# Kernel tuning notes

Measured on AMD Instinct MI355X. Metric: run time of the kernel, lower is better.

## Reference

```python
import jax, jax.numpy as jnp
import numpy as np

N_EMBD = 1024
HEAD_SIZE = 64  # n_embd // n_head = 1024 // 16


def setup_inputs() -> dict:
    key = jax.random.key(0)
    ks = jax.random.split(key, 7)
    B, T, C, H = 4, 2048, N_EMBD, HEAD_SIZE
    s = 1.0 / np.sqrt(C)
    return {
        "x": jax.random.normal(ks[0], (B, T, C), dtype=jnp.float32),
        "Wq": jax.random.normal(ks[1], (C, H), dtype=jnp.float32) * s,
        "bq": jax.random.normal(ks[2], (H,), dtype=jnp.float32) * 0.01,
        "Wk": jax.random.normal(ks[3], (C, H), dtype=jnp.float32) * s,
        "bk": jax.random.normal(ks[4], (H,), dtype=jnp.float32) * 0.01,
        "Wv": jax.random.normal(ks[5], (C, H), dtype=jnp.float32) * s,
        "bv": jax.random.normal(ks[6], (H,), dtype=jnp.float32) * 0.01,
    }


def reference(x, Wq, bq, Wk, bk, Wv, bv):
    # x: [B, T, C]
    B, T, C = x.shape
    q = x @ Wq + bq  # [B, T, H]
    k = x @ Wk + bk  # [B, T, H]
    v = x @ Wv + bv  # [B, T, H]
    # NOTE: original module does NOT scale by 1/sqrt(head_size)
    wei = jnp.einsum("bth,bsh->bts", q, k)  # [B, T, T]
    causal = jnp.tril(jnp.ones((T, T), dtype=bool))
    wei = jnp.where(causal, wei, -jnp.inf)
    wei = jax.nn.softmax(wei, axis=-1)
    out = jnp.einsum("bts,bsh->bth", wei, v)  # [B, T, H]
    return out
```

## Files before the change

kernel.cpp:

```cpp
#include <hip/hip_runtime.h>

typedef float f32x4 __attribute__((ext_vector_type(4)));
typedef short s16x4 __attribute__((ext_vector_type(4)));
typedef short s16x8 __attribute__((ext_vector_type(8)));

#define LOG2E 1.4426950408889634f

__device__ __forceinline__ short f2bf(float f) {
  unsigned u = __float_as_uint(f);
  unsigned r = (u + 0x7fffu + ((u >> 16) & 1u)) >> 16;
  return (short)r;
}
__device__ __forceinline__ float bf2f(short s) {
  return __uint_as_float(((unsigned)(unsigned short)s) << 16);
}
__device__ __forceinline__ unsigned cvt_pk_bf16(float a, float b) {
  unsigned r;
  asm("v_cvt_pk_bf16_f32 %0, %1, %2" : "=v"(r) : "v"(a), "v"(b));
  return r;
}

__device__ __forceinline__ f32x4 mfma16(s16x4 a, s16x4 b, f32x4 c) {
  return __builtin_amdgcn_mfma_f32_16x16x16bf16_1k(a, b, c, 0, 0, 0);
}
__device__ __forceinline__ f32x4 mfma32(s16x8 a, s16x8 b, f32x4 c) {
  return __builtin_amdgcn_mfma_f32_16x16x32_bf16(a, b, c, 0, 0, 0);
}

__device__ __forceinline__ void gl_lds16(const void* gp, void* sp) {
  __builtin_amdgcn_global_load_lds(
      (__attribute__((address_space(1))) void*)const_cast<void*>(gp),
      (__attribute__((address_space(3))) void*)sp, 16, 0, 0);
}

__global__ __launch_bounds__(256) void prep_w(
    const float* __restrict__ Wq, const float* __restrict__ Wk, const float* __restrict__ Wv,
    short* __restrict__ wt_hi, short* __restrict__ wt_lo) {
  int idx = blockIdx.x * 256 + threadIdx.x;
  int n = idx >> 10;
  int c = idx & 1023;
  const float* W = (n < 64) ? Wq : ((n < 128) ? Wk : Wv);
  float v = W[c * 64 + (n & 63)];
  short hi = f2bf(v);
  short lo = f2bf(v - bf2f(hi));
  wt_hi[idx] = hi;
  wt_lo[idx] = lo;
}

__global__ __launch_bounds__(512, 2) void proj_qkv(
    const float* __restrict__ x,
    const short* __restrict__ wt_hi, const short* __restrict__ wt_lo,
    const float* __restrict__ bq, const float* __restrict__ bk, const float* __restrict__ bv,
    short* __restrict__ q_hi, short* __restrict__ q_lo,
    short* __restrict__ k_hi, short* __restrict__ k_lo,
    short* __restrict__ v_t) {
  const int tid = threadIdx.x;
  const int lane = tid & 63;
  const int wv = tid >> 6;
  const int col = lane & 15;
  const int g = lane >> 4;
  const int mg = wv >> 2;
  const int ng = wv & 3;
  const int tokbase = blockIdx.x * 32;

  __shared__ short lds[5][12288];

  const int wsl = ((lane & 3) ^ ((lane >> 3) & 3)) * 8;
  const short* s0 = wt_hi + (size_t)(16 * wv + (lane >> 2)) * 1024 + wsl;
  const int d0 = wv * 512;
  const int c1 = wv + 8;
  const short* s1 = (c1 < 12 ? wt_hi + (size_t)(16 * c1 + (lane >> 2)) * 1024
                             : wt_lo + (size_t)(16 * (c1 - 12) + (lane >> 2)) * 1024) + wsl;
  const int d1 = (c1 < 12) ? c1 * 512 : 6144 + (c1 - 12) * 512;
  const int c2 = wv + 16;
  const bool isx = (c2 >= 20);
  const short* s2 = isx
      ? (const short*)(x + (size_t)(tokbase + 8 * (c2 - 20) + (lane >> 3)) * 1024 +
                       ((lane & 7) ^ (lane >> 3)) * 4)
      : wt_lo + (size_t)(16 * (c2 - 12) + (lane >> 2)) * 1024 + wsl;
  const int d2 = isx ? 10240 + (c2 - 20) * 512 : 6144 + (c2 - 12) * 512;
  const int st2 = isx ? 64 : 32;

#define STAGE(BP, S) do { \
    gl_lds16(s0 + (S) * 32, (BP) + d0); \
    gl_lds16(s1 + (S) * 32, (BP) + d1); \
    gl_lds16(s2 + (S) * st2, (BP) + d2); \
  } while (0)

#define PIPE_WAIT(N) do { \
    asm volatile("s_waitcnt vmcnt(" #N ")" ::: "memory"); \
    __builtin_amdgcn_s_barrier(); \
    __builtin_amdgcn_sched_barrier(0); \
  } while (0)
#define PIPE_END do { \
    asm volatile("s_waitcnt lgkmcnt(0)" ::: "memory"); \
    __builtin_amdgcn_sched_barrier(0); \
    __builtin_amdgcn_s_barrier(); \
  } while (0)

  const int arow = mg * 16 + col;
  const int xq0 = ((2 * g) ^ (arow & 7)) << 2;
  const int xq1 = ((2 * g + 1) ^ (arow & 7)) << 2;
  const int rq = ng * 16 + col;
  const int ws = (g ^ ((rq >> 1) & 3)) << 3;

  f32x4 accQ = {0,0,0,0}, accK = {0,0,0,0}, accV = {0,0,0,0};

  typedef union { unsigned u[4]; s16x8 v8; } pk8;

#define COMPUTE(BP) do { \
    const short* bp_ = (BP); \
    const float* xb_ = (const float*)(bp_ + 10240); \
    f32x4 x0_ = *(const f32x4*)(xb_ + arow * 32 + xq0); \
    f32x4 x1_ = *(const f32x4*)(xb_ + arow * 32 + xq1); \
    pk8 xh_, xl_; \
    xh_.u[0] = cvt_pk_bf16(x0_[0], x0_[1]); \
    xh_.u[1] = cvt_pk_bf16(x0_[2], x0_[3]); \
    xh_.u[2] = cvt_pk_bf16(x1_[0], x1_[1]); \
    xh_.u[3] = cvt_pk_bf16(x1_[2], x1_[3]); \
    xl_.u[0] = cvt_pk_bf16(x0_[0] - __uint_as_float(xh_.u[0] << 16), \
                           x0_[1] - __uint_as_float(xh_.u[0] & 0xffff0000u)); \
    xl_.u[1] = cvt_pk_bf16(x0_[2] - __uint_as_float(xh_.u[1] << 16), \
                           x0_[3] - __uint_as_float(xh_.u[1] & 0xffff0000u)); \
    xl_.u[2] = cvt_pk_bf16(x1_[0] - __uint_as_float(xh_.u[2] << 16), \
                           x1_[1] - __uint_as_float(xh_.u[2] & 0xffff0000u)); \
    xl_.u[3] = cvt_pk_bf16(x1_[2] - __uint_as_float(xh_.u[3] << 16), \
                           x1_[3] - __uint_as_float(xh_.u[3] & 0xffff0000u)); \
    s16x8 qh_ = *(const s16x8*)(bp_ + rq * 32 + ws); \
    s16x8 kh_ = *(const s16x8*)(bp_ + (64 + rq) * 32 + ws); \
    s16x8 vh_ = *(const s16x8*)(bp_ + (128 + rq) * 32 + ws); \
    s16x8 ql_ = *(const s16x8*)(bp_ + 6144 + rq * 32 + ws); \
    s16x8 kl_ = *(const s16x8*)(bp_ + 6144 + (64 + rq) * 32 + ws); \
    accQ = mfma32(xh_.v8, qh_, accQ); \
    accK = mfma32(xh_.v8, kh_, accK); \
    accV = mfma32(xh_.v8, vh_, accV); \
    accQ = mfma32(xl_.v8, qh_, accQ); \
    accK = mfma32(xl_.v8, kh_, accK); \
    accQ = mfma32(xh_.v8, ql_, accQ); \
    accK = mfma32(xh_.v8, kl_, accK); \
  } while (0)

  short* cA = &lds[0][0];
  short* cB = &lds[1][0];
  short* cC = &lds[2][0];
  short* cD = &lds[3][0];
  short* cE = &lds[4][0];

  STAGE(cA, 0); STAGE(cB, 1); STAGE(cC, 2); STAGE(cD, 3);

#pragma unroll 1
  for (int b = 0; b < 28; ++b) {
    STAGE(cE, b + 4);
    PIPE_WAIT(12);
    COMPUTE(cA);
    PIPE_END;
    short* t = cA; cA = cB; cB = cC; cC = cD; cD = cE; cE = t;
  }
  PIPE_WAIT(9); COMPUTE(cA); PIPE_END;
  PIPE_WAIT(6); COMPUTE(cB); PIPE_END;
  PIPE_WAIT(3); COMPUTE(cC); PIPE_END;
  PIPE_WAIT(0); COMPUTE(cD);

  {
    const int hQ = ng * 16 + col;
    const float biasq = bq[hQ];
    const float biask = bk[hQ];
    const float biasv = bv[hQ];
#pragma unroll
    for (int r = 0; r < 4; ++r) {
      const int tok = tokbase + mg * 16 + 4 * g + r;
      float fq = accQ[r] + biasq;
      short qh = f2bf(fq);
      q_hi[(size_t)tok * 64 + hQ] = qh;
      q_lo[(size_t)tok * 64 + hQ] = f2bf(fq - bf2f(qh));
      float fk = accK[r] + biask;
      short kh = f2bf(fk);
      k_hi[(size_t)tok * 64 + hQ] = kh;
      k_lo[(size_t)tok * 64 + hQ] = f2bf(fk - bf2f(kh));
      const int bb = tok >> 11;
      const int tl = tok & 2047;
      v_t[((size_t)bb * 64 + hQ) * 2048 + tl] = f2bf(accV[r] + biasv);
    }
  }
#undef STAGE
#undef PIPE_WAIT
#undef PIPE_END
#undef COMPUTE
}

__global__ __launch_bounds__(512, 2) void attn(
    const short* __restrict__ q_hi, const short* __restrict__ q_lo,
    const short* __restrict__ k_hi, const short* __restrict__ k_lo,
    const short* __restrict__ v_t,
    float* __restrict__ pm, float* __restrict__ pl, float* __restrict__ pO) {
  const int tid = threadIdx.x;
  const int lane = tid & 63;
  const int w = tid >> 6;
  const int col = lane & 15;
  const int g = lane >> 4;
  const int bid = blockIdx.x;
  const int p = bid & 7;
  const int b = (bid >> 3) & 3;
  const int s = bid >> 5;
  if (s > p) return;

  __shared__ short lds[3][12288];

  const int qlo = 256 * p + 32 * w;
  const int kb0 = 256 * s;

  const short* qbh = q_hi + (size_t)(b * 2048 + qlo + col) * 64 + g * 8;
  const short* qbl = q_lo + (size_t)(b * 2048 + qlo + col) * 64 + g * 8;
  s16x8 qh0a = *(const s16x8*)(qbh);
  s16x8 qh1a = *(const s16x8*)(qbh + 32);
  s16x8 ql0a = *(const s16x8*)(qbl);
  s16x8 ql1a = *(const s16x8*)(qbl + 32);
  s16x8 qh0b = *(const s16x8*)(qbh + 16 * 64);
  s16x8 qh1b = *(const s16x8*)(qbh + 16 * 64 + 32);
  s16x8 ql0b = *(const s16x8*)(qbl + 16 * 64);
  s16x8 ql1b = *(const s16x8*)(qbl + 16 * 64 + 32);
  asm volatile("s_waitcnt vmcnt(0)" ::: "memory");
  __builtin_amdgcn_sched_barrier(0);

  f32x4 oA0 = {0,0,0,0}, oA1 = {0,0,0,0}, oA2 = {0,0,0,0}, oA3 = {0,0,0,0};
  f32x4 oB0 = {0,0,0,0}, oB1 = {0,0,0,0}, oB2 = {0,0,0,0}, oB3 = {0,0,0,0};
  float mA = -3.0e38f, lA = 0.0f, mB = -3.0e38f, lB = 0.0f;

#define STAGE(BP, J) do { \
    const int kbs_ = kb0 + 64 * (J); \
    const int r_ = 8 * w + (lane >> 3); \
    const int lc_ = (lane & 7) ^ (lane >> 3); \
    gl_lds16(k_hi + (size_t)(b * 2048 + kbs_ + r_) * 64 + lc_ * 8, (BP) + 8 * w * 64); \
    gl_lds16(k_lo + (size_t)(b * 2048 + kbs_ + r_) * 64 + lc_ * 8, (BP) + 4096 + 8 * w * 64); \
    gl_lds16(v_t + ((size_t)b * 64 + r_) * 2048 + kbs_ + lc_ * 8, (BP) + 8192 + 8 * w * 64); \
  } while (0)

#define PIPE_WAIT(N) do { \
    asm volatile("s_waitcnt vmcnt(" #N ")" ::: "memory"); \
    __builtin_amdgcn_s_barrier(); \
    __builtin_amdgcn_sched_barrier(0); \
  } while (0)
#define PIPE_END do { \
    asm volatile("s_waitcnt lgkmcnt(0)" ::: "memory"); \
    __builtin_amdgcn_sched_barrier(0); \
    __builtin_amdgcn_s_barrier(); \
  } while (0)

#define TILE_U(Qh0, Qh1, Ql0, Ql1, mX, lX, O0, O1, O2, O3, DIAG) do { \
    f32x4 u1_ = {0,0,0,0}, u2_ = {0,0,0,0}; \
    u1_ = mfma32(kh0_, Qh0, u1_); u1_ = mfma32(kh1_, Qh1, u1_); \
    u2_ = mfma32(kh0_, Ql0, u2_); u2_ = mfma32(kh1_, Ql1, u2_); \
    u2_ = mfma32(kl0_, Qh0, u2_); u2_ = mfma32(kl1_, Qh1, u2_); \
    f32x4 s_ = u1_ + u2_; \
    if (kg0_ == (DIAG)) { \
      _Pragma("unroll") for (int i = 0; i < 4; ++i) \
        if (4 * g + i > col) s_[i] = -3.0e38f; \
    } \
    float mx_ = fmaxf(fmaxf(s_[0], s_[1]), fmaxf(s_[2], s_[3])); \
    mx_ = fmaxf(mx_, __shfl_xor(mx_, 16)); \
    mx_ = fmaxf(mx_, __shfl_xor(mx_, 32)); \
    if (!__all(mx_ <= mX + 8.0f)) { \
      const float mn_ = fmaxf(mX, mx_); \
      const float rs_ = __builtin_amdgcn_exp2f((mX - mn_) * LOG2E); \
      lX *= rs_; O0 *= rs_; O1 *= rs_; O2 *= rs_; O3 *= rs_; \
      mX = mn_; \
    } \
    const float p0_ = __builtin_amdgcn_exp2f((s_[0] - mX) * LOG2E); \
    const float p1_ = __builtin_amdgcn_exp2f((s_[1] - mX) * LOG2E); \
    const float p2_ = __builtin_amdgcn_exp2f((s_[2] - mX) * LOG2E); \
    const float p3_ = __builtin_amdgcn_exp2f((s_[3] - mX) * LOG2E); \
    lX += p0_ + p1_ + p2_ + p3_; \
    s16x4 pb_; \
    pb_[0] = f2bf(p0_); pb_[1] = f2bf(p1_); pb_[2] = f2bf(p2_); pb_[3] = f2bf(p3_); \
    O0 = mfma16(v0_, pb_, O0); \
    O1 = mfma16(v1_, pb_, O1); \
    O2 = mfma16(v2_, pb_, O2); \
    O3 = mfma16(v3_, pb_, O3); \
  } while (0)

#define STEP_U(U) do { \
    const int kg0_ = kb_ + 16 * U; \
    if (kg0_ <= qlo + 31) { \
      const int cx_ = col & 7; \
      const short* kr_ = bp_ + (16 * U + col) * 64; \
      s16x8 kh0_ = *(const s16x8*)(kr_ + ((g ^ cx_) << 3)); \
      s16x8 kh1_ = *(const s16x8*)(kr_ + (((4 + g) ^ cx_) << 3)); \
      s16x8 kl0_ = *(const s16x8*)(kr_ + 4096 + ((g ^ cx_) << 3)); \
      s16x8 kl1_ = *(const s16x8*)(kr_ + 4096 + (((4 + g) ^ cx_) << 3)); \
      const short* vr_ = bp_ + 8192 + col * 64 + ((g & 1) << 2) + \
                         (((2 * U + (g >> 1)) ^ cx_) << 3); \
      s16x4 v0_ = *(const s16x4*)(vr_); \
      s16x4 v1_ = *(const s16x4*)(vr_ + 1024); \
      s16x4 v2_ = *(const s16x4*)(vr_ + 2048); \
      s16x4 v3_ = *(const s16x4*)(vr_ + 3072); \
      TILE_U(qh0b, qh1b, ql0b, ql1b, mB, lB, oB0, oB1, oB2, oB3, qlo + 16); \
      if (kg0_ <= qlo + 15) \
        TILE_U(qh0a, qh1a, ql0a, ql1a, mA, lA, oA0, oA1, oA2, oA3, qlo); \
    } \
  } while (0)

#define COMPUTE(BP, J) do { \
    const int kb_ = kb0 + 64 * (J); \
    if (kb_ <= qlo + 31) { \
      const short* bp_ = (BP); \
      STEP_U(0); STEP_U(1); STEP_U(2); STEP_U(3); \
    } \
  } while (0)

  short* L0 = &lds[0][0];
  short* L1 = &lds[1][0];
  short* L2 = &lds[2][0];

  STAGE(L0, 0); STAGE(L1, 1);
  STAGE(L2, 2); PIPE_WAIT(6); COMPUTE(L0, 0); PIPE_END;
  STAGE(L0, 3); PIPE_WAIT(6); COMPUTE(L1, 1); PIPE_END;
  PIPE_WAIT(3); COMPUTE(L2, 2); PIPE_END;
  PIPE_WAIT(0); COMPUTE(L0, 3);

  lA += __shfl_xor(lA, 16); lA += __shfl_xor(lA, 32);
  lB += __shfl_xor(lB, 16); lB += __shfl_xor(lB, 32);
  const int rowA = b * 2048 + qlo + col;
  const int rowB = rowA + 16;
  if (g == 0) {
    pm[s * 8192 + rowA] = mA;  pl[s * 8192 + rowA] = lA;
    pm[s * 8192 + rowB] = mB;  pl[s * 8192 + rowB] = lB;
  }
  {
    float* dA = pO + ((size_t)s * 8192 + rowA) * 64 + 4 * g;
    float* dB = pO + ((size_t)s * 8192 + rowB) * 64 + 4 * g;
    *(f32x4*)(dA)      = oA0; *(f32x4*)(dA + 16) = oA1;
    *(f32x4*)(dA + 32) = oA2; *(f32x4*)(dA + 48) = oA3;
    *(f32x4*)(dB)      = oB0; *(f32x4*)(dB + 16) = oB1;
    *(f32x4*)(dB + 32) = oB2; *(f32x4*)(dB + 48) = oB3;
  }
#undef STAGE
#undef PIPE_WAIT
#undef PIPE_END
#undef TILE_U
#undef STEP_U
#undef COMPUTE
}

__global__ __launch_bounds__(256) void reduce_p(
    const float* __restrict__ pm, const float* __restrict__ pl,
    const float* __restrict__ pO, float* __restrict__ out) {
  const int idx = blockIdx.x * 256 + threadIdx.x;
  const int row = idx >> 4;
  const int hq = (idx & 15) * 4;
  const int smax = (row & 2047) >> 8;
  float M = -3.0e38f;
  for (int s = 0; s <= smax; ++s) M = fmaxf(M, pm[s * 8192 + row]);
  float L = 0.f;
  f32x4 acc = {0, 0, 0, 0};
  for (int s = 0; s <= smax; ++s) {
    const float ws = __builtin_amdgcn_exp2f((pm[s * 8192 + row] - M) * LOG2E);
    L += ws * pl[s * 8192 + row];
    f32x4 ov = *(const f32x4*)(pO + ((size_t)s * 8192 + row) * 64 + hq);
    acc += ov * ws;
  }
  const float invL = 1.0f / L;
  *(f32x4*)(out + (size_t)row * 64 + hq) = acc * invL;
}

extern "C" void kernel_launch(void* const* d_in, const int* in_sizes, int n_in,
                              void* d_out, int out_size, void* d_ws, size_t ws_size,
                              hipStream_t stream) {
  const float* x  = (const float*)d_in[0];
  const float* Wq = (const float*)d_in[1];
  const float* bq = (const float*)d_in[2];
  const float* Wk = (const float*)d_in[3];
  const float* bk = (const float*)d_in[4];
  const float* Wv = (const float*)d_in[5];
  const float* bv = (const float*)d_in[6];
  float* out = (float*)d_out;

  char* ws = (char*)d_ws;
  short* wt_hi = (short*)(ws);
  short* wt_lo = (short*)(ws + 393216);
  short* q_hi  = (short*)(ws + 786432);
  short* q_lo  = (short*)(ws + 786432 + 1048576);
  short* k_hi  = (short*)(ws + 786432 + 2 * 1048576);
  short* k_lo  = (short*)(ws + 786432 + 3 * 1048576);
  short* v_t   = (short*)(ws + 786432 + 4 * 1048576);
  float* pm    = (float*)(ws + 6029312);
  float* pl    = (float*)(ws + 6291456);
  float* pO    = (float*)(ws + 6553600);

  hipLaunchKernelGGL(prep_w, dim3(768), dim3(256), 0, stream, Wq, Wk, Wv, wt_hi, wt_lo);
  hipLaunchKernelGGL(proj_qkv, dim3(256), dim3(512), 0, stream,
                     x, wt_hi, wt_lo, bq, bk, bv, q_hi, q_lo, k_hi, k_lo, v_t);
  hipLaunchKernelGGL(attn, dim3(256), dim3(512), 0, stream,
                     q_hi, q_lo, k_hi, k_lo, v_t, pm, pl, pO);
  hipLaunchKernelGGL(reduce_p, dim3(512), dim3(256), 0, stream, pm, pl, pO, out);
}
```

Before: 56.72 us.

## Restructure attention into 64-row query blocks with 512-key splits and looped pipeline

```diff
diff --git a/kernel.cpp b/kernel.cpp
--- a/kernel.cpp
+++ b/kernel.cpp
@@ -188,7 +188,7 @@
 #undef COMPUTE
 }
 
-__global__ __launch_bounds__(512, 2) void attn(
+__global__ __launch_bounds__(256, 3) void attn(
     const short* __restrict__ q_hi, const short* __restrict__ q_lo,
     const short* __restrict__ k_hi, const short* __restrict__ k_lo,
     const short* __restrict__ v_t,
@@ -199,40 +199,46 @@
   const int col = lane & 15;
   const int g = lane >> 4;
   const int bid = blockIdx.x;
-  const int p = bid & 7;
-  const int b = (bid >> 3) & 3;
-  const int s = bid >> 5;
-  if (s > p) return;
-
-  __shared__ short lds[3][12288];
-
-  const int qlo = 256 * p + 32 * w;
-  const int kb0 = 256 * s;
+  const int p = bid & 31;
+  const int b = (bid >> 5) & 3;
+  const int s = bid >> 7;
+  const int kb0 = 512 * s;
+  if (kb0 > 64 * p + 63) return;
+  const int S = (((64 * p + 63 - kb0) >> 5) + 1) < 16
+                    ? (((64 * p + 63 - kb0) >> 5) + 1) : 16;
+
+  __shared__ short lds[4][6144];
+
+  const int qlo = 64 * p + 16 * w;
 
   const short* qbh = q_hi + (size_t)(b * 2048 + qlo + col) * 64 + g * 8;
   const short* qbl = q_lo + (size_t)(b * 2048 + qlo + col) * 64 + g * 8;
-  s16x8 qh0a = *(const s16x8*)(qbh);
-  s16x8 qh1a = *(const s16x8*)(qbh + 32);
-  s16x8 ql0a = *(const s16x8*)(qbl);
-  s16x8 ql1a = *(const s16x8*)(qbl + 32);
-  s16x8 qh0b = *(const s16x8*)(qbh + 16 * 64);
-  s16x8 qh1b = *(const s16x8*)(qbh + 16 * 64 + 32);
-  s16x8 ql0b = *(const s16x8*)(qbl + 16 * 64);
-  s16x8 ql1b = *(const s16x8*)(qbl + 16 * 64 + 32);
+  s16x8 qh0 = *(const s16x8*)(qbh);
+  s16x8 qh1 = *(const s16x8*)(qbh + 32);
+  s16x8 ql0 = *(const s16x8*)(qbl);
+  s16x8 ql1 = *(const s16x8*)(qbl + 32);
   asm volatile("s_waitcnt vmcnt(0)" ::: "memory");
   __builtin_amdgcn_sched_barrier(0);
-
-  f32x4 oA0 = {0,0,0,0}, oA1 = {0,0,0,0}, oA2 = {0,0,0,0}, oA3 = {0,0,0,0};
-  f32x4 oB0 = {0,0,0,0}, oB1 = {0,0,0,0}, oB2 = {0,0,0,0}, oB3 = {0,0,0,0};
-  float mA = -3.0e38f, lA = 0.0f, mB = -3.0e38f, lB = 0.0f;
-
-#define STAGE(BP, J) do { \
-    const int kbs_ = kb0 + 64 * (J); \
-    const int r_ = 8 * w + (lane >> 3); \
-    const int lc_ = (lane & 7) ^ (lane >> 3); \
-    gl_lds16(k_hi + (size_t)(b * 2048 + kbs_ + r_) * 64 + lc_ * 8, (BP) + 8 * w * 64); \
-    gl_lds16(k_lo + (size_t)(b * 2048 + kbs_ + r_) * 64 + lc_ * 8, (BP) + 4096 + 8 * w * 64); \
-    gl_lds16(v_t + ((size_t)b * 64 + r_) * 2048 + kbs_ + lc_ * 8, (BP) + 8192 + 8 * w * 64); \
+  asm volatile("" : "+v"(qh0), "+v"(qh1), "+v"(ql0), "+v"(ql1));
+
+  f32x4 o0 = {0,0,0,0}, o1 = {0,0,0,0}, o2 = {0,0,0,0}, o3 = {0,0,0,0};
+  float m = -3.0e38f, l = 0.0f;
+
+  const int kr32 = 8 * w + (lane >> 3);
+  const int ksl = ((lane & 7) ^ (lane >> 3)) * 8;
+  const short* khs = k_hi + (size_t)(b * 2048 + kb0 + kr32) * 64 + ksl;
+  const short* kls = k_lo + (size_t)(b * 2048 + kb0 + kr32) * 64 + ksl;
+  const int vh_r = 16 * w + (lane >> 2);
+  const int vsl = ((2 * (lane & 3)) ^ (vh_r & 6)) * 4;
+  const short* vs = v_t + ((size_t)b * 64 + vh_r) * 2048 + kb0 + vsl;
+  const int kdst = kr32 * 64;
+  const int vdst = 4096 + vh_r * 32 - (lane >> 2) * 32 + (lane & 15) * 8;
+
+#define STAGE(J) do { \
+    short* bp_ = &lds[(J) & 3][0]; \
+    gl_lds16(khs + (J) * 32 * 64, bp_ + w * 512); \
+    gl_lds16(kls + (J) * 32 * 64, bp_ + 2048 + w * 512); \
+    gl_lds16(vs + (J) * 32, bp_ + 4096 + w * 512); \
   } while (0)
 
 #define PIPE_WAIT(N) do { \
@@ -246,98 +252,89 @@
     __builtin_amdgcn_s_barrier(); \
   } while (0)
 
-#define TILE_U(Qh0, Qh1, Ql0, Ql1, mX, lX, O0, O1, O2, O3, DIAG) do { \
+  const int cx = col & 7;
+  const int kslot0 = (g ^ cx) << 3;
+  const int kslot1 = ((4 + g) ^ cx) << 3;
+  const int vg0 = ((g) ^ (col & 6)) << 2;
+  const int vg1 = ((4 + g) ^ (col & 6)) << 2;
+
+#define SUBTILE(BP, KG0, VGOFF) do { \
+    const short* kr_ = (BP) + ((KG0)&31) * 64 + col * 64; \
+    s16x8 kh0_ = *(const s16x8*)(kr_ + kslot0); \
+    s16x8 kh1_ = *(const s16x8*)(kr_ + kslot1); \
+    s16x8 kl0_ = *(const s16x8*)(kr_ + 2048 + kslot0); \
+    s16x8 kl1_ = *(const s16x8*)(kr_ + 2048 + kslot1); \
     f32x4 u1_ = {0,0,0,0}, u2_ = {0,0,0,0}; \
-    u1_ = mfma32(kh0_, Qh0, u1_); u1_ = mfma32(kh1_, Qh1, u1_); \
-    u2_ = mfma32(kh0_, Ql0, u2_); u2_ = mfma32(kh1_, Ql1, u2_); \
-    u2_ = mfma32(kl0_, Qh0, u2_); u2_ = mfma32(kl1_, Qh1, u2_); \
+    u1_ = mfma32(kh0_, qh0, u1_); u1_ = mfma32(kh1_, qh1, u1_); \
+    u2_ = mfma32(kh0_, ql0, u2_); u2_ = mfma32(kh1_, ql1, u2_); \
+    u2_ = mfma32(kl0_, qh0, u2_); u2_ = mfma32(kl1_, qh1, u2_); \
     f32x4 s_ = u1_ + u2_; \
-    if (kg0_ == (DIAG)) { \
+    if ((KG0) == qlo) { \
       _Pragma("unroll") for (int i = 0; i < 4; ++i) \
         if (4 * g + i > col) s_[i] = -3.0e38f; \
     } \
     float mx_ = fmaxf(fmaxf(s_[0], s_[1]), fmaxf(s_[2], s_[3])); \
     mx_ = fmaxf(mx_, __shfl_xor(mx_, 16)); \
     mx_ = fmaxf(mx_, __shfl_xor(mx_, 32)); \
-    if (!__all(mx_ <= mX + 8.0f)) { \
-      const float mn_ = fmaxf(mX, mx_); \
-      const float rs_ = __builtin_amdgcn_exp2f((mX - mn_) * LOG2E); \
-      lX *= rs_; O0 *= rs_; O1 *= rs_; O2 *= rs_; O3 *= rs_; \
-      mX = mn_; \
-    } \
-    const float p0_ = __builtin_amdgcn_exp2f((s_[0] - mX) * LOG2E); \
-    const float p1_ = __builtin_amdgcn_exp2f((s_[1] - mX) * LOG2E); \
-    const float p2_ = __builtin_amdgcn_exp2f((s_[2] - mX) * LOG2E); \
-    const float p3_ = __builtin_amdgcn_exp2f((s_[3] - mX) * LOG2E); \
-    lX += p0_ + p1_ + p2_ + p3_; \
+    const float mn_ = fmaxf(m, mx_); \
+    const float rs_ = __builtin_amdgcn_exp2f((m - mn_) * LOG2E); \
+    const float p0_ = __builtin_amdgcn_exp2f((s_[0] - mn_) * LOG2E); \
+    const float p1_ = __builtin_amdgcn_exp2f((s_[1] - mn_) * LOG2E); \
+    const float p2_ = __builtin_amdgcn_exp2f((s_[2] - mn_) * LOG2E); \
+    const float p3_ = __builtin_amdgcn_exp2f((s_[3] - mn_) * LOG2E); \
+    l = l * rs_ + (p0_ + p1_ + p2_ + p3_); \
+    o0 *= rs_; o1 *= rs_; o2 *= rs_; o3 *= rs_; \
+    m = mn_; \
     s16x4 pb_; \
     pb_[0] = f2bf(p0_); pb_[1] = f2bf(p1_); pb_[2] = f2bf(p2_); pb_[3] = f2bf(p3_); \
-    O0 = mfma16(v0_, pb_, O0); \
-    O1 = mfma16(v1_, pb_, O1); \
-    O2 = mfma16(v2_, pb_, O2); \
-    O3 = mfma16(v3_, pb_, O3); \
-  } while (0)
-
-#define STEP_U(U) do { \
-    const int kg0_ = kb_ + 16 * U; \
-    if (kg0_ <= qlo + 31) { \
-      const int cx_ = col & 7; \
-      const short* kr_ = bp_ + (16 * U + col) * 64; \
-      s16x8 kh0_ = *(const s16x8*)(kr_ + ((g ^ cx_) << 3)); \
-      s16x8 kh1_ = *(const s16x8*)(kr_ + (((4 + g) ^ cx_) << 3)); \
-      s16x8 kl0_ = *(const s16x8*)(kr_ + 4096 + ((g ^ cx_) << 3)); \
-      s16x8 kl1_ = *(const s16x8*)(kr_ + 4096 + (((4 + g) ^ cx_) << 3)); \
-      const short* vr_ = bp_ + 8192 + col * 64 + ((g & 1) << 2) + \
-                         (((2 * U + (g >> 1)) ^ cx_) << 3); \
-      s16x4 v0_ = *(const s16x4*)(vr_); \
-      s16x4 v1_ = *(const s16x4*)(vr_ + 1024); \
-      s16x4 v2_ = *(const s16x4*)(vr_ + 2048); \
-      s16x4 v3_ = *(const s16x4*)(vr_ + 3072); \
-      TILE_U(qh0b, qh1b, ql0b, ql1b, mB, lB, oB0, oB1, oB2, oB3, qlo + 16); \
-      if (kg0_ <= qlo + 15) \
-        TILE_U(qh0a, qh1a, ql0a, ql1a, mA, lA, oA0, oA1, oA2, oA3, qlo); \
+    const short* vb_ = (BP) + 4096 + col * 32 + (VGOFF); \
+    o0 = mfma16(*(const s16x4*)(vb_),        pb_, o0); \
+    o1 = mfma16(*(const s16x4*)(vb_ + 512),  pb_, o1); \
+    o2 = mfma16(*(const s16x4*)(vb_ + 1024), pb_, o2); \
+    o3 = mfma16(*(const s16x4*)(vb_ + 1536), pb_, o3); \
+  } while (0)
+
+#define COMPUTE(J) do { \
+    const int kb_ = kb0 + 32 * (J); \
+    if (kb_ <= qlo + 15) { \
+      short* bp_ = &lds[(J) & 3][0]; \
+      SUBTILE(bp_, kb_, vg0); \
+      if (kb_ + 16 <= qlo + 15) SUBTILE(bp_, kb_ + 16, vg1); \
     } \
   } while (0)
 
-#define COMPUTE(BP, J) do { \
-    const int kb_ = kb0 + 64 * (J); \
-    if (kb_ <= qlo + 31) { \
-      const short* bp_ = (BP); \
-      STEP_U(0); STEP_U(1); STEP_U(2); STEP_U(3); \
-    } \
-  } while (0)
-
-  short* L0 = &lds[0][0];
-  short* L1 = &lds[1][0];
-  short* L2 = &lds[2][0];
-
-  STAGE(L0, 0); STAGE(L1, 1);
-  STAGE(L2, 2); PIPE_WAIT(6); COMPUTE(L0, 0); PIPE_END;
-  STAGE(L0, 3); PIPE_WAIT(6); COMPUTE(L1, 1); PIPE_END;
-  PIPE_WAIT(3); COMPUTE(L2, 2); PIPE_END;
-  PIPE_WAIT(0); COMPUTE(L0, 3);
-
-  lA += __shfl_xor(lA, 16); lA += __shfl_xor(lA, 32);
-  lB += __shfl_xor(lB, 16); lB += __shfl_xor(lB, 32);
-  const int rowA = b * 2048 + qlo + col;
-  const int rowB = rowA + 16;
+  STAGE(0); STAGE(1);
+  if (S > 2) STAGE(2);
+
+#pragma unroll 1
+  for (int j = 0; j + 3 < S; ++j) {
+    STAGE(j + 3);
+    PIPE_WAIT(9);
+    COMPUTE(j);
+    PIPE_END;
+  }
+  if (S >= 3) { PIPE_WAIT(6); COMPUTE(S - 3); PIPE_END; }
+  PIPE_WAIT(3); COMPUTE(S - 2); PIPE_END;
+  PIPE_WAIT(0); COMPUTE(S - 1);
+
+  l += __shfl_xor(l, 16);
+  l += __shfl_xor(l, 32);
+  const int row = b * 2048 + qlo + col;
   if (g == 0) {
-    pm[s * 8192 + rowA] = mA;  pl[s * 8192 + rowA] = lA;
-    pm[s * 8192 + rowB] = mB;  pl[s * 8192 + rowB] = lB;
+    pm[s * 8192 + row] = m;
+    pl[s * 8192 + row] = l;
   }
   {
-    float* dA = pO + ((size_t)s * 8192 + rowA) * 64 + 4 * g;
-    float* dB = pO + ((size_t)s * 8192 + rowB) * 64 + 4 * g;
-    *(f32x4*)(dA)      = oA0; *(f32x4*)(dA + 16) = oA1;
-    *(f32x4*)(dA + 32) = oA2; *(f32x4*)(dA + 48) = oA3;
-    *(f32x4*)(dB)      = oB0; *(f32x4*)(dB + 16) = oB1;
-    *(f32x4*)(dB + 32) = oB2; *(f32x4*)(dB + 48) = oB3;
+    float* d = pO + ((size_t)s * 8192 + row) * 64 + 4 * g;
+    *(f32x4*)(d)      = o0;
+    *(f32x4*)(d + 16) = o1;
+    *(f32x4*)(d + 32) = o2;
+    *(f32x4*)(d + 48) = o3;
   }
 #undef STAGE
 #undef PIPE_WAIT
 #undef PIPE_END
-#undef TILE_U
-#undef STEP_U
+#undef SUBTILE
 #undef COMPUTE
 }
 
@@ -347,7 +344,7 @@
   const int idx = blockIdx.x * 256 + threadIdx.x;
   const int row = idx >> 4;
   const int hq = (idx & 15) * 4;
-  const int smax = (row & 2047) >> 8;
+  const int smax = (row & 2047) >> 9;
   float M = -3.0e38f;
   for (int s = 0; s <= smax; ++s) M = fmaxf(M, pm[s * 8192 + row]);
   float L = 0.f;
@@ -383,13 +380,13 @@
   short* k_lo  = (short*)(ws + 786432 + 3 * 1048576);
   short* v_t   = (short*)(ws + 786432 + 4 * 1048576);
   float* pm    = (float*)(ws + 6029312);
-  float* pl    = (float*)(ws + 6291456);
-  float* pO    = (float*)(ws + 6553600);
+  float* pl    = (float*)(ws + 6160384);
+  float* pO    = (float*)(ws + 6291456);
 
   hipLaunchKernelGGL(prep_w, dim3(768), dim3(256), 0, stream, Wq, Wk, Wv, wt_hi, wt_lo);
   hipLaunchKernelGGL(proj_qkv, dim3(256), dim3(512), 0, stream,
                      x, wt_hi, wt_lo, bq, bk, bv, q_hi, q_lo, k_hi, k_lo, v_t);
-  hipLaunchKernelGGL(attn, dim3(256), dim3(512), 0, stream,
+  hipLaunchKernelGGL(attn, dim3(512), dim3(256), 0, stream,
                      q_hi, q_lo, k_hi, k_lo, v_t, pm, pl, pO);
   hipLaunchKernelGGL(reduce_p, dim3(512), dim3(256), 0, stream, pm, pl, pO, out);
 }
```

Result: faster. 54.60 us (-3.7%).
